# Kernel optimization log

Measured on AMD Instinct MI355X. Metric: run time of the kernel, lower is better.

## Reference

```python
import jax, jax.numpy as jnp
import numpy as np

BN_EPS = 1e-5
INTERP_EPS = 1e-8


def _bn_relu(x, g, b, m, v):
    # eval-mode BatchNorm1d over channel dim (last axis here) + ReLU
    return jax.nn.relu((x - m) * (g / jnp.sqrt(v + BN_EPS)) + b)


def setup_inputs() -> dict:
    key = jax.random.key(0)
    ks = jax.random.split(key, 12)
    B, N, S, C1, C2 = 4, 16384, 1024, 128, 256
    Cin = C1 + C2  # 384
    H1, H2 = 256, 128
    inp = {
        "xyz1": jax.random.normal(ks[0], (B, N, 3), jnp.float32),
        "xyz2": jax.random.normal(ks[1], (B, S, 3), jnp.float32),
        "points1": jax.random.normal(ks[2], (B, N, C1), jnp.float32),
        "points2": jax.random.normal(ks[3], (B, S, C2), jnp.float32),
        # Conv1d(k=1, bias=False) weights: (out_ch, in_ch)
        "w1": jax.random.normal(ks[4], (H1, Cin), jnp.float32) * (1.0 / np.sqrt(Cin)),
        "g1": jax.random.uniform(ks[5], (H1,), jnp.float32, 0.5, 1.5),
        "b1": jax.random.normal(ks[6], (H1,), jnp.float32) * 0.1,
        "m1": jax.random.normal(ks[7], (H1,), jnp.float32) * 0.1,
        "v1": jax.random.uniform(ks[8], (H1,), jnp.float32, 0.5, 1.5),
        "w2": jax.random.normal(ks[9], (H2, H1), jnp.float32) * (1.0 / np.sqrt(H1)),
        "g2": jax.random.uniform(ks[10], (H2,), jnp.float32, 0.5, 1.5),
        "b2": jax.random.normal(ks[11], (H2,), jnp.float32) * 0.1,
        "m2": jnp.zeros((H2,), jnp.float32),
        "v2": jnp.ones((H2,), jnp.float32),
    }
    return inp


def reference(xyz1, xyz2, points1, points2, w1, g1, b1, m1, v1, w2, g2, b2, m2, v2):
    B, N, _ = xyz1.shape
    S = xyz2.shape[1]
    # squared pairwise distances (B, N, S) via ||a||^2 + ||b||^2 - 2 a.b
    sq = (
        jnp.sum(xyz1 * xyz1, -1)[:, :, None]
        + jnp.sum(xyz2 * xyz2, -1)[:, None, :]
        - 2.0 * jnp.einsum("bnd,bsd->bns", xyz1, xyz2)
    )
    neg_d, idx = jax.lax.top_k(-sq, 3)  # 3 nearest neighbors
    dists = -neg_d  # (B, N, 3) squared distances, ascending
    recip = 1.0 / (dists + INTERP_EPS)
    weight = recip / jnp.sum(recip, -1, keepdims=True)  # (B, N, 3)
    # gather neighbor features: (B, N, 3, C2)
    gathered = points2[jnp.arange(B)[:, None, None], idx]
    interpolated = jnp.einsum("bnk,bnkc->bnc", weight, gathered)
    new_points = jnp.concatenate([points1, interpolated], axis=-1)  # (B, N, Cin)
    h = _bn_relu(jnp.einsum("bnc,dc->bnd", new_points, w1), g1, b1, m1, v1)
    out = _bn_relu(jnp.einsum("bnc,dc->bnd", h, w2), g2, b2, m2, v2)
    return out
```

## Files before the change

kernel.cpp:

```cpp
#include <hip/hip_runtime.h>
#include <math.h>

#define B_    4
#define N_    16384
#define S_    1024
#define C1_   128
#define C2_   256
#define CIN_  384
#define H1_   256
#define H2_   128
#define BN_EPS_     1e-5f
#define INTERP_EPS_ 1e-8f

typedef _Float16 f16;
typedef _Float16 f16x4 __attribute__((ext_vector_type(4)));
typedef _Float16 f16x8 __attribute__((ext_vector_type(8)));
typedef float    f32x4 __attribute__((ext_vector_type(4)));
typedef unsigned int u32;

#define GLD16(g, l) \
  __builtin_amdgcn_global_load_lds((const __attribute__((address_space(1))) void*)(g), \
                                   (__attribute__((address_space(3))) void*)(l), 16, 0, 0)

#define WS_XI   1048576
#define WS_W1F  68157440
#define WS_W2F  68354048
#define WS_SC1  68419584
#define WS_SH1  68420608
#define WS_SC2  68421632
#define WS_SH2  68422144

__device__ __forceinline__ u32 umin_(u32 a, u32 b) { return a < b ? a : b; }
__device__ __forceinline__ u32 umax_(u32 a, u32 b) { return a > b ? a : b; }

#define KINS(k) do { \
    u32 c1 = umax_(s0, (k)); s0 = umin_(s0, (k)); \
    u32 c2 = umax_(s1, c1);  s1 = umin_(s1, c1);  \
    u32 c3 = umax_(s2, c2);  s2 = umin_(s2, c2);  \
    u32 c4 = umax_(s3, c3);  s3 = umin_(s3, c3);  \
    s4 = umin_(s4, c4); } while (0)

#define CSWAP(a_, b_) do { \
    if (rd[b_] < rd[a_] || (rd[b_] == rd[a_] && ri[b_] < ri[a_])) { \
      double td = rd[a_]; rd[a_] = rd[b_]; rd[b_] = td; \
      int ti = ri[a_]; ri[a_] = ri[b_]; ri[b_] = ti; } } while (0)

__global__ __launch_bounds__(256) void front_kernel(
    const float* __restrict__ xyz1, const float* __restrict__ xyz2,
    const float* __restrict__ points2,
    const float* __restrict__ w1, const float* __restrict__ w2,
    const float* __restrict__ g1, const float* __restrict__ b1,
    const float* __restrict__ m1, const float* __restrict__ v1,
    const float* __restrict__ g2, const float* __restrict__ b2,
    const float* __restrict__ m2, const float* __restrict__ v2,
    f16* __restrict__ xi, f16* __restrict__ w1f, f16* __restrict__ w2f,
    float* __restrict__ sc1, float* __restrict__ sh1,
    float* __restrict__ sc2, float* __restrict__ sh2)
{
    const int bid = blockIdx.x;
    const int t   = threadIdx.x;

    if (bid >= 2048) {
        const int tg = (bid - 2048) * 256 + t;
        if (tg < 98304) {
            w1f[tg] = (f16)w1[tg];
        } else if (tg < 131072) {
            w2f[tg - 98304] = (f16)w2[tg - 98304];
        } else if (tg < 131328) {
            const int c = tg - 131072;
            const float s = g1[c] / sqrtf(v1[c] + BN_EPS_);
            sc1[c] = s; sh1[c] = b1[c] - m1[c] * s;
        } else if (tg < 131456) {
            const int c = tg - 131328;
            const float s = g2[c] / sqrtf(v2[c] + BN_EPS_);
            sc2[c] = s; sh2[c] = b2[c] - m2[c] * s;
        }
        return;
    }

    __shared__ float4 q[S_ + 8];
    __shared__ int   idr[32][3];
    __shared__ float wtr[32][3];

    const int b     = bid >> 9;
    const int pbase = (bid & 511) << 5;

    for (int i = t; i < S_; i += 256) {
        const float* s = &xyz2[((size_t)b * S_ + i) * 3];
        float4 v; v.x = s[0]; v.y = s[1]; v.z = s[2]; v.w = 0.0f;
        q[i + (i >> 7)] = v;
    }
    __syncthreads();

    {
        const int p     = pbase + (t >> 3);
        const int chunk = t & 7;
        const int qb    = chunk * 129;
        const int ebase = chunk << 7;
        const float* pp = &xyz1[((size_t)b * N_ + p) * 3];
        const float px = pp[0], py = pp[1], pz = pp[2];

        u32 s0 = 0xFFFFFFFFu, s1 = 0xFFFFFFFFu, s2 = 0xFFFFFFFFu,
            s3 = 0xFFFFFFFFu, s4 = 0xFFFFFFFFu;

        for (int i = 0; i < 128; i += 4) {
            #pragma unroll
            for (int u = 0; u < 4; ++u) {
                const float4 c = q[qb + i + u];
                const float dx = px - c.x, dy = py - c.y, dz = pz - c.z;
                const float dd = fmaf(dx, dx, fmaf(dy, dy, dz * dz));
                const u32 k = (__float_as_uint(dd) & 0xFFFFFC00u) | (u32)(ebase + i + u);
                KINS(k);
            }
        }
        #pragma unroll
        for (int msk = 1; msk <= 4; msk <<= 1) {
            u32 e0 = __shfl_xor(s0, msk), e1 = __shfl_xor(s1, msk);
            u32 e2 = __shfl_xor(s2, msk), e3 = __shfl_xor(s3, msk);
            u32 e4 = __shfl_xor(s4, msk);
            KINS(e0); KINS(e1); KINS(e2); KINS(e3); KINS(e4);
        }
        if (chunk == 0) {
            const double px6 = px, py6 = py, pz6 = pz;
            double rd[5]; int ri[5];
            const u32 ks[5] = {s0, s1, s2, s3, s4};
            #pragma unroll
            for (int j = 0; j < 5; ++j) {
                const int si = (int)(ks[j] & 1023u); ri[j] = si;
                const float4 c = q[si + (si >> 7)];
                const double dx = px6 - (double)c.x, dy = py6 - (double)c.y, dz = pz6 - (double)c.z;
                rd[j] = dx * dx + dy * dy + dz * dz;
            }
            CSWAP(0,1); CSWAP(1,2); CSWAP(0,1); CSWAP(2,3); CSWAP(1,2);
            CSWAP(0,1); CSWAP(3,4); CSWAP(2,3); CSWAP(1,2); CSWAP(0,1);
            const float r0 = 1.0f / ((float)rd[0] + INTERP_EPS_);
            const float r1 = 1.0f / ((float)rd[1] + INTERP_EPS_);
            const float r2 = 1.0f / ((float)rd[2] + INTERP_EPS_);
            const float rs = r0 + r1 + r2;
            const int r = t >> 3;
            idr[r][0] = ri[0]; idr[r][1] = ri[1]; idr[r][2] = ri[2];
            wtr[r][0] = r0 / rs; wtr[r][1] = r1 / rs; wtr[r][2] = r2 / rs;
        }
    }
    __syncthreads();

    {
        const int r = t >> 3, j = t & 7;
        const int i0 = idr[r][0], i1 = idr[r][1], i2 = idr[r][2];
        const float w0 = wtr[r][0], w1w = wtr[r][1], w2w = wtr[r][2];
        const float* p2b = points2 + (size_t)b * S_ * C2_;
        const int c0 = j * 32;
        float a[32];
        #pragma unroll
        for (int g = 0; g < 8; ++g) {
            const float4 f = *(const float4*)&p2b[i0 * C2_ + c0 + g * 4];
            a[g*4+0] = w0 * f.x; a[g*4+1] = w0 * f.y; a[g*4+2] = w0 * f.z; a[g*4+3] = w0 * f.w;
        }
        #pragma unroll
        for (int g = 0; g < 8; ++g) {
            const float4 f = *(const float4*)&p2b[i1 * C2_ + c0 + g * 4];
            a[g*4+0] = fmaf(w1w, f.x, a[g*4+0]); a[g*4+1] = fmaf(w1w, f.y, a[g*4+1]);
            a[g*4+2] = fmaf(w1w, f.z, a[g*4+2]); a[g*4+3] = fmaf(w1w, f.w, a[g*4+3]);
        }
        #pragma unroll
        for (int g = 0; g < 8; ++g) {
            const float4 f = *(const float4*)&p2b[i2 * C2_ + c0 + g * 4];
            a[g*4+0] = fmaf(w2w, f.x, a[g*4+0]); a[g*4+1] = fmaf(w2w, f.y, a[g*4+1]);
            a[g*4+2] = fmaf(w2w, f.z, a[g*4+2]); a[g*4+3] = fmaf(w2w, f.w, a[g*4+3]);
        }
        const size_t grow = (size_t)(b * N_ + pbase + r);
        #pragma unroll
        for (int g8 = 0; g8 < 4; ++g8) {
            f16x8 o;
            #pragma unroll
            for (int e = 0; e < 8; ++e) o[e] = (f16)a[g8 * 8 + e];
            *(f16x8*)&xi[grow * C2_ + c0 + g8 * 8] = o;
        }
    }
}

__device__ __forceinline__ void mfma_step1(const f16* As, const f16* Bs,
                                           f32x4 (&acc)[4][8],
                                           int wr, int wc, int lrow, int lhi)
{
    f16x8 af[4], bf[8];
    #pragma unroll
    for (int m = 0; m < 4; ++m)
        af[m] = *(const f16x8*)&As[(wr * 64 + m * 16 + lrow) * 32 + lhi * 8];
    #pragma unroll
    for (int n = 0; n < 8; ++n)
        bf[n] = *(const f16x8*)&Bs[(wc * 128 + n * 16 + lrow) * 32 + lhi * 8];
    #pragma unroll
    for (int m = 0; m < 4; ++m)
        #pragma unroll
        for (int n = 0; n < 8; ++n)
            acc[m][n] = __builtin_amdgcn_mfma_f32_16x16x32_f16(af[m], bf[n], acc[m][n], 0, 0, 0);
}

__global__ __launch_bounds__(256, 2) void mlp_kernel(
    const float* __restrict__ points1, const f16* __restrict__ xi,
    const f16* __restrict__ w1f, const f16* __restrict__ w2f,
    const float* __restrict__ sc1v, const float* __restrict__ sh1v,
    const float* __restrict__ sc2v, const float* __restrict__ sh2v,
    float* __restrict__ out)
{
    extern __shared__ __align__(16) char smem[];
    f16* As = (f16*)smem;
    f16* Bs = (f16*)(smem + 16384);
    char* Ht = smem + 16384;

    const int t = threadIdx.x;
    const int w = t >> 6;
    const int lane = t & 63;
    const int wr = w >> 1, wc = w & 1;
    const int lrow = lane & 15, lhi = lane >> 4;
    const int rowbase = blockIdx.x * 128;

    const int srow = t >> 1, khalf = t & 1;
    const float* p1r = points1 + (size_t)(rowbase + srow) * C1_;

    f32x4 acc[4][8] = {};
    float4 pre0, pre1, pre2, pre3;

    {
        const float* src = p1r + khalf * 16;
        pre0 = *(const float4*)(src + 0);
        pre1 = *(const float4*)(src + 4);
        pre2 = *(const float4*)(src + 8);
        pre3 = *(const float4*)(src + 12);
        f16* asrow = As + srow * 32 + khalf * 16;
        f16x4 o0 = {(f16)pre0.x, (f16)pre0.y, (f16)pre0.z, (f16)pre0.w};
        f16x4 o1 = {(f16)pre1.x, (f16)pre1.y, (f16)pre1.z, (f16)pre1.w};
        f16x4 o2 = {(f16)pre2.x, (f16)pre2.y, (f16)pre2.z, (f16)pre2.w};
        f16x4 o3 = {(f16)pre3.x, (f16)pre3.y, (f16)pre3.z, (f16)pre3.w};
        *(f16x4*)(asrow + 0) = o0; *(f16x4*)(asrow + 4) = o1;
        *(f16x4*)(asrow + 8) = o2; *(f16x4*)(asrow + 12) = o3;
        #pragma unroll
        for (int j = 0; j < 4; ++j) {
            const int c = j * 256 + t;
            GLD16(w1f + (size_t)(c >> 2) * CIN_ + (c & 3) * 8,
                  (char*)Bs + (j * 4096 + w * 1024));
        }
    }
    __syncthreads();

    for (int step = 0; step < 12; ++step) {
        const int pb = step & 1, nb = pb ^ 1;
        const int nkb = (step + 1) * 32;
        const bool has_next = (step < 11);
        const bool nextA = (nkb < C1_);

        if (has_next) {
            if (nextA) {
                const float* src = p1r + nkb + khalf * 16;
                pre0 = *(const float4*)(src + 0);
                pre1 = *(const float4*)(src + 4);
                pre2 = *(const float4*)(src + 8);
                pre3 = *(const float4*)(src + 12);
            } else {
                const int kk = nkb - C1_;
                #pragma unroll
                for (int j = 0; j < 2; ++j) {
                    const int c = j * 256 + t;
                    GLD16(xi + (size_t)(rowbase + (c >> 2)) * C2_ + kk + (c & 3) * 8,
                          (char*)As + (nb * 8192 + j * 4096 + w * 1024));
                }
            }
            #pragma unroll
            for (int j = 0; j < 4; ++j) {
                const int c = j * 256 + t;
                GLD16(w1f + (size_t)(c >> 2) * CIN_ + nkb + (c & 3) * 8,
                      (char*)Bs + (nb * 16384 + j * 4096 + w * 1024));
            }
        }

        mfma_step1(As + pb * 4096, Bs + pb * 8192, acc, wr, wc, lrow, lhi);

        if (has_next && nextA) {
            f16* asrow = As + nb * 4096 + srow * 32 + khalf * 16;
            f16x4 o0 = {(f16)pre0.x, (f16)pre0.y, (f16)pre0.z, (f16)pre0.w};
            f16x4 o1 = {(f16)pre1.x, (f16)pre1.y, (f16)pre1.z, (f16)pre1.w};
            f16x4 o2 = {(f16)pre2.x, (f16)pre2.y, (f16)pre2.z, (f16)pre2.w};
            f16x4 o3 = {(f16)pre3.x, (f16)pre3.y, (f16)pre3.z, (f16)pre3.w};
            *(f16x4*)(asrow + 0) = o0; *(f16x4*)(asrow + 4) = o1;
            *(f16x4*)(asrow + 8) = o2; *(f16x4*)(asrow + 12) = o3;
        }
        __syncthreads();
    }

    #pragma unroll
    for (int j = 0; j < 2; ++j) {
        const int c = j * 256 + t;
        GLD16(w2f + (size_t)(c >> 2) * H1_ + (c & 3) * 8,
              smem + (j * 4096 + w * 1024));
    }
    #pragma unroll
    for (int n = 0; n < 8; ++n) {
        const int col = wc * 128 + n * 16 + lrow;
        const float sc = sc1v[col], sh = sh1v[col];
        #pragma unroll
        for (int m = 0; m < 4; ++m) {
            #pragma unroll
            for (int i = 0; i < 4; ++i) {
                const int row = wr * 64 + m * 16 + lhi * 4 + i;
                const float v = fmaxf(fmaf(acc[m][n][i], sc, sh), 0.0f);
                const u32 byteoff = (u32)(row * 512 + col * 2) ^ ((u32)(row & 7) << 4);
                *(f16*)(Ht + byteoff) = (f16)v;
            }
        }
    }
    __syncthreads();

    f32x4 acc2[4][4] = {};
    for (int step = 0; step < 8; ++step) {
        const int pb = step & 1, nb = pb ^ 1;
        const int nkb = (step + 1) * 32;
        if (step < 7) {
            #pragma unroll
            for (int j = 0; j < 2; ++j) {
                const int c = j * 256 + t;
                GLD16(w2f + (size_t)(c >> 2) * H1_ + nkb + (c & 3) * 8,
                      smem + (nb * 8192 + j * 4096 + w * 1024));
            }
        }
        f16x8 af[4], bf[4];
        #pragma unroll
        for (int m = 0; m < 4; ++m) {
            const int row = wr * 64 + m * 16 + lrow;
            const u32 byteoff = (u32)(row * 512 + (step * 32 + lhi * 8) * 2) ^ ((u32)(row & 7) << 4);
            af[m] = *(const f16x8*)(Ht + byteoff);
        }
        const f16* Bc = (const f16*)(smem + pb * 8192);
        #pragma unroll
        for (int n = 0; n < 4; ++n)
            bf[n] = *(const f16x8*)&Bc[(wc * 64 + n * 16 + lrow) * 32 + lhi * 8];
        #pragma unroll
        for (int m = 0; m < 4; ++m)
            #pragma unroll
            for (int n = 0; n < 4; ++n)
                acc2[m][n] = __builtin_amdgcn_mfma_f32_16x16x32_f16(af[m], bf[n], acc2[m][n], 0, 0, 0);
        __syncthreads();
    }

    #pragma unroll
    for (int n = 0; n < 4; ++n) {
        const int col = wc * 64 + n * 16 + lrow;
        const float sc = sc2v[col], sh = sh2v[col];
        #pragma unroll
        for (int m = 0; m < 4; ++m) {
            const int row0 = rowbase + wr * 64 + m * 16 + lhi * 4;
            #pragma unroll
            for (int i = 0; i < 4; ++i) {
                out[(size_t)(row0 + i) * H2_ + col] = fmaxf(fmaf(acc2[m][n][i], sc, sh), 0.0f);
            }
        }
    }
}

extern "C" void kernel_launch(void* const* d_in, const int* in_sizes, int n_in,
                              void* d_out, int out_size, void* d_ws, size_t ws_size,
                              hipStream_t stream) {
    const float* xyz1    = (const float*)d_in[0];
    const float* xyz2    = (const float*)d_in[1];
    const float* points1 = (const float*)d_in[2];
    const float* points2 = (const float*)d_in[3];
    const float* w1      = (const float*)d_in[4];
    const float* g1      = (const float*)d_in[5];
    const float* b1      = (const float*)d_in[6];
    const float* m1      = (const float*)d_in[7];
    const float* v1      = (const float*)d_in[8];
    const float* w2      = (const float*)d_in[9];
    const float* g2      = (const float*)d_in[10];
    const float* b2      = (const float*)d_in[11];
    const float* m2      = (const float*)d_in[12];
    const float* v2      = (const float*)d_in[13];
    float* out = (float*)d_out;

    char* ws = (char*)d_ws;
    f16*   xi_ws = (f16*)(ws + WS_XI);
    f16*   w1f   = (f16*)(ws + WS_W1F);
    f16*   w2f   = (f16*)(ws + WS_W2F);
    float* sc1   = (float*)(ws + WS_SC1);
    float* sh1   = (float*)(ws + WS_SH1);
    float* sc2   = (float*)(ws + WS_SC2);
    float* sh2   = (float*)(ws + WS_SH2);

    front_kernel<<<dim3(2562), dim3(256), 0, stream>>>(
        xyz1, xyz2, points2, w1, w2, g1, b1, m1, v1, g2, b2, m2, v2,
        xi_ws, w1f, w2f, sc1, sh1, sc2, sh2);
    mlp_kernel<<<dim3(512), dim3(256), 81920, stream>>>(
        points1, xi_ws, w1f, w2f, sc1, sh1, sc2, sh2, out);
}
```

Baseline: 183.9 us.

## Halve MLP row tile and widen KNN per-thread scan range

The front kernel now handles 64 query points per block, with 4 threads per point each scanning 256 candidates instead of 8 threads scanning 128, so fewer blocks reload xyz2 into shared memory and the top-k merge needs fewer shuffle rounds. The MLP kernel drops from 128 to 64 rows per block, cutting shared memory from 80KB to 48KB and accumulators in half so three blocks can fit per CU, and the grid doubles to 1024 blocks. The trade-off is that each W1/W2 tile loaded from global memory is reused across fewer rows, and the longer serial scan per thread in the KNN phase gives less parallelism per point.

```diff
diff --git a/kernel.cpp b/kernel.cpp
--- a/kernel.cpp
+++ b/kernel.cpp
@@ -60,8 +60,8 @@
     const int bid = blockIdx.x;
     const int t   = threadIdx.x;
 
-    if (bid >= 2048) {
-        const int tg = (bid - 2048) * 256 + t;
+    if (bid >= 1024) {
+        const int tg = (bid - 1024) * 256 + t;
         if (tg < 98304) {
             w1f[tg] = (f16)w1[tg];
         } else if (tg < 131072) {
@@ -78,32 +78,32 @@
         return;
     }
 
-    __shared__ float4 q[S_ + 8];
-    __shared__ int   idr[32][3];
-    __shared__ float wtr[32][3];
-
-    const int b     = bid >> 9;
-    const int pbase = (bid & 511) << 5;
+    __shared__ float4 q[S_ + 4];
+    __shared__ int   idr[64][3];
+    __shared__ float wtr[64][3];
+
+    const int b     = bid >> 8;
+    const int pbase = (bid & 255) << 6;
 
     for (int i = t; i < S_; i += 256) {
         const float* s = &xyz2[((size_t)b * S_ + i) * 3];
         float4 v; v.x = s[0]; v.y = s[1]; v.z = s[2]; v.w = 0.0f;
-        q[i + (i >> 7)] = v;
+        q[i + (i >> 8)] = v;
     }
     __syncthreads();
 
     {
-        const int p     = pbase + (t >> 3);
-        const int chunk = t & 7;
-        const int qb    = chunk * 129;
-        const int ebase = chunk << 7;
+        const int p     = pbase + (t >> 2);
+        const int chunk = t & 3;
+        const int qb    = chunk * 257;
+        const int ebase = chunk << 8;
         const float* pp = &xyz1[((size_t)b * N_ + p) * 3];
         const float px = pp[0], py = pp[1], pz = pp[2];
 
         u32 s0 = 0xFFFFFFFFu, s1 = 0xFFFFFFFFu, s2 = 0xFFFFFFFFu,
             s3 = 0xFFFFFFFFu, s4 = 0xFFFFFFFFu;
 
-        for (int i = 0; i < 128; i += 4) {
+        for (int i = 0; i < 256; i += 4) {
             #pragma unroll
             for (int u = 0; u < 4; ++u) {
                 const float4 c = q[qb + i + u];
@@ -114,7 +114,7 @@
             }
         }
         #pragma unroll
-        for (int msk = 1; msk <= 4; msk <<= 1) {
+        for (int msk = 1; msk <= 2; msk <<= 1) {
             u32 e0 = __shfl_xor(s0, msk), e1 = __shfl_xor(s1, msk);
             u32 e2 = __shfl_xor(s2, msk), e3 = __shfl_xor(s3, msk);
             u32 e4 = __shfl_xor(s4, msk);
@@ -127,7 +127,7 @@
             #pragma unroll
             for (int j = 0; j < 5; ++j) {
                 const int si = (int)(ks[j] & 1023u); ri[j] = si;
-                const float4 c = q[si + (si >> 7)];
+                const float4 c = q[si + (si >> 8)];
                 const double dx = px6 - (double)c.x, dy = py6 - (double)c.y, dz = pz6 - (double)c.z;
                 rd[j] = dx * dx + dy * dy + dz * dz;
             }
@@ -137,15 +137,16 @@
             const float r1 = 1.0f / ((float)rd[1] + INTERP_EPS_);
             const float r2 = 1.0f / ((float)rd[2] + INTERP_EPS_);
             const float rs = r0 + r1 + r2;
-            const int r = t >> 3;
+            const int r = t >> 2;
             idr[r][0] = ri[0]; idr[r][1] = ri[1]; idr[r][2] = ri[2];
             wtr[r][0] = r0 / rs; wtr[r][1] = r1 / rs; wtr[r][2] = r2 / rs;
         }
     }
     __syncthreads();
 
-    {
-        const int r = t >> 3, j = t & 7;
+    #pragma unroll
+    for (int rr = 0; rr < 64; rr += 32) {
+        const int r = (t >> 3) + rr, j = t & 7;
         const int i0 = idr[r][0], i1 = idr[r][1], i2 = idr[r][2];
         const float w0 = wtr[r][0], w1w = wtr[r][1], w2w = wtr[r][2];
         const float* p2b = points2 + (size_t)b * S_ * C2_;
@@ -179,25 +180,7 @@
     }
 }
 
-__device__ __forceinline__ void mfma_step1(const f16* As, const f16* Bs,
-                                           f32x4 (&acc)[4][8],
-                                           int wr, int wc, int lrow, int lhi)
-{
-    f16x8 af[4], bf[8];
-    #pragma unroll
-    for (int m = 0; m < 4; ++m)
-        af[m] = *(const f16x8*)&As[(wr * 64 + m * 16 + lrow) * 32 + lhi * 8];
-    #pragma unroll
-    for (int n = 0; n < 8; ++n)
-        bf[n] = *(const f16x8*)&Bs[(wc * 128 + n * 16 + lrow) * 32 + lhi * 8];
-    #pragma unroll
-    for (int m = 0; m < 4; ++m)
-        #pragma unroll
-        for (int n = 0; n < 8; ++n)
-            acc[m][n] = __builtin_amdgcn_mfma_f32_16x16x32_f16(af[m], bf[n], acc[m][n], 0, 0, 0);
-}
-
-__global__ __launch_bounds__(256, 2) void mlp_kernel(
+__global__ __launch_bounds__(256, 3) void mlp_kernel(
     const float* __restrict__ points1, const f16* __restrict__ xi,
     const f16* __restrict__ w1f, const f16* __restrict__ w2f,
     const float* __restrict__ sc1v, const float* __restrict__ sh1v,
@@ -206,7 +189,7 @@
 {
     extern __shared__ __align__(16) char smem[];
     f16* As = (f16*)smem;
-    f16* Bs = (f16*)(smem + 16384);
+    f16* Bs = (f16*)(smem + 8192);
     char* Ht = smem + 16384;
 
     const int t = threadIdx.x;
@@ -214,27 +197,22 @@
     const int lane = t & 63;
     const int wr = w >> 1, wc = w & 1;
     const int lrow = lane & 15, lhi = lane >> 4;
-    const int rowbase = blockIdx.x * 128;
-
-    const int srow = t >> 1, khalf = t & 1;
+    const int rowbase = blockIdx.x * 64;
+
+    const int srow = t >> 2, kq = t & 3;
     const float* p1r = points1 + (size_t)(rowbase + srow) * C1_;
 
-    f32x4 acc[4][8] = {};
-    float4 pre0, pre1, pre2, pre3;
+    f32x4 acc[2][8] = {};
+    float4 pre0, pre1;
 
     {
-        const float* src = p1r + khalf * 16;
+        const float* src = p1r + kq * 8;
         pre0 = *(const float4*)(src + 0);
         pre1 = *(const float4*)(src + 4);
-        pre2 = *(const float4*)(src + 8);
-        pre3 = *(const float4*)(src + 12);
-        f16* asrow = As + srow * 32 + khalf * 16;
+        f16* asrow = As + srow * 32 + kq * 8;
         f16x4 o0 = {(f16)pre0.x, (f16)pre0.y, (f16)pre0.z, (f16)pre0.w};
         f16x4 o1 = {(f16)pre1.x, (f16)pre1.y, (f16)pre1.z, (f16)pre1.w};
-        f16x4 o2 = {(f16)pre2.x, (f16)pre2.y, (f16)pre2.z, (f16)pre2.w};
-        f16x4 o3 = {(f16)pre3.x, (f16)pre3.y, (f16)pre3.z, (f16)pre3.w};
         *(f16x4*)(asrow + 0) = o0; *(f16x4*)(asrow + 4) = o1;
-        *(f16x4*)(asrow + 8) = o2; *(f16x4*)(asrow + 12) = o3;
         #pragma unroll
         for (int j = 0; j < 4; ++j) {
             const int c = j * 256 + t;
@@ -252,19 +230,13 @@
 
         if (has_next) {
             if (nextA) {
-                const float* src = p1r + nkb + khalf * 16;
+                const float* src = p1r + nkb + kq * 8;
                 pre0 = *(const float4*)(src + 0);
                 pre1 = *(const float4*)(src + 4);
-                pre2 = *(const float4*)(src + 8);
-                pre3 = *(const float4*)(src + 12);
             } else {
                 const int kk = nkb - C1_;
-                #pragma unroll
-                for (int j = 0; j < 2; ++j) {
-                    const int c = j * 256 + t;
-                    GLD16(xi + (size_t)(rowbase + (c >> 2)) * C2_ + kk + (c & 3) * 8,
-                          (char*)As + (nb * 8192 + j * 4096 + w * 1024));
-                }
+                GLD16(xi + (size_t)(rowbase + (t >> 2)) * C2_ + kk + (t & 3) * 8,
+                      (char*)As + (nb * 4096 + w * 1024));
             }
             #pragma unroll
             for (int j = 0; j < 4; ++j) {
@@ -274,16 +246,28 @@
             }
         }
 
-        mfma_step1(As + pb * 4096, Bs + pb * 8192, acc, wr, wc, lrow, lhi);
+        {
+            const f16* Ac = As + pb * 2048;
+            const f16* Bc = Bs + pb * 8192;
+            f16x8 af[2], bf[8];
+            #pragma unroll
+            for (int m = 0; m < 2; ++m)
+                af[m] = *(const f16x8*)&Ac[(wr * 32 + m * 16 + lrow) * 32 + lhi * 8];
+            #pragma unroll
+            for (int n = 0; n < 8; ++n)
+                bf[n] = *(const f16x8*)&Bc[(wc * 128 + n * 16 + lrow) * 32 + lhi * 8];
+            #pragma unroll
+            for (int m = 0; m < 2; ++m)
+                #pragma unroll
+                for (int n = 0; n < 8; ++n)
+                    acc[m][n] = __builtin_amdgcn_mfma_f32_16x16x32_f16(af[m], bf[n], acc[m][n], 0, 0, 0);
+        }
 
         if (has_next && nextA) {
-            f16* asrow = As + nb * 4096 + srow * 32 + khalf * 16;
+            f16* asrow = As + nb * 2048 + srow * 32 + kq * 8;
             f16x4 o0 = {(f16)pre0.x, (f16)pre0.y, (f16)pre0.z, (f16)pre0.w};
             f16x4 o1 = {(f16)pre1.x, (f16)pre1.y, (f16)pre1.z, (f16)pre1.w};
-            f16x4 o2 = {(f16)pre2.x, (f16)pre2.y, (f16)pre2.z, (f16)pre2.w};
-            f16x4 o3 = {(f16)pre3.x, (f16)pre3.y, (f16)pre3.z, (f16)pre3.w};
             *(f16x4*)(asrow + 0) = o0; *(f16x4*)(asrow + 4) = o1;
-            *(f16x4*)(asrow + 8) = o2; *(f16x4*)(asrow + 12) = o3;
         }
         __syncthreads();
     }
@@ -299,10 +283,10 @@
         const int col = wc * 128 + n * 16 + lrow;
         const float sc = sc1v[col], sh = sh1v[col];
         #pragma unroll
-        for (int m = 0; m < 4; ++m) {
+        for (int m = 0; m < 2; ++m) {
             #pragma unroll
             for (int i = 0; i < 4; ++i) {
-                const int row = wr * 64 + m * 16 + lhi * 4 + i;
+                const int row = wr * 32 + m * 16 + lhi * 4 + i;
                 const float v = fmaxf(fmaf(acc[m][n][i], sc, sh), 0.0f);
                 const u32 byteoff = (u32)(row * 512 + col * 2) ^ ((u32)(row & 7) << 4);
                 *(f16*)(Ht + byteoff) = (f16)v;
@@ -311,7 +295,7 @@
     }
     __syncthreads();
 
-    f32x4 acc2[4][4] = {};
+    f32x4 acc2[2][4] = {};
     for (int step = 0; step < 8; ++step) {
         const int pb = step & 1, nb = pb ^ 1;
         const int nkb = (step + 1) * 32;
@@ -323,10 +307,10 @@
                       smem + (nb * 8192 + j * 4096 + w * 1024));
             }
         }
-        f16x8 af[4], bf[4];
-        #pragma unroll
-        for (int m = 0; m < 4; ++m) {
-            const int row = wr * 64 + m * 16 + lrow;
+        f16x8 af[2], bf[4];
+        #pragma unroll
+        for (int m = 0; m < 2; ++m) {
+            const int row = wr * 32 + m * 16 + lrow;
             const u32 byteoff = (u32)(row * 512 + (step * 32 + lhi * 8) * 2) ^ ((u32)(row & 7) << 4);
             af[m] = *(const f16x8*)(Ht + byteoff);
         }
@@ -335,7 +319,7 @@
         for (int n = 0; n < 4; ++n)
             bf[n] = *(const f16x8*)&Bc[(wc * 64 + n * 16 + lrow) * 32 + lhi * 8];
         #pragma unroll
-        for (int m = 0; m < 4; ++m)
+        for (int m = 0; m < 2; ++m)
             #pragma unroll
             for (int n = 0; n < 4; ++n)
                 acc2[m][n] = __builtin_amdgcn_mfma_f32_16x16x32_f16(af[m], bf[n], acc2[m][n], 0, 0, 0);
@@ -347,8 +331,8 @@
         const int col = wc * 64 + n * 16 + lrow;
         const float sc = sc2v[col], sh = sh2v[col];
         #pragma unroll
-        for (int m = 0; m < 4; ++m) {
-            const int row0 = rowbase + wr * 64 + m * 16 + lhi * 4;
+        for (int m = 0; m < 2; ++m) {
+            const int row0 = rowbase + wr * 32 + m * 16 + lhi * 4;
             #pragma unroll
             for (int i = 0; i < 4; ++i) {
                 out[(size_t)(row0 + i) * H2_ + col] = fmaxf(fmaf(acc2[m][n][i], sc, sh), 0.0f);
@@ -385,9 +369,9 @@
     float* sc2   = (float*)(ws + WS_SC2);
     float* sh2   = (float*)(ws + WS_SH2);
 
-    front_kernel<<<dim3(2562), dim3(256), 0, stream>>>(
+    front_kernel<<<dim3(1538), dim3(256), 0, stream>>>(
         xyz1, xyz2, points2, w1, w2, g1, b1, m1, v1, g2, b2, m2, v2,
         xi_ws, w1f, w2f, sc1, sh1, sc2, sh2);
-    mlp_kernel<<<dim3(512), dim3(256), 81920, stream>>>(
+    mlp_kernel<<<dim3(1024), dim3(256), 49152, stream>>>(
         points1, xi_ws, w1f, w2f, sc1, sh1, sc2, sh2, out);
 }
```

Result: slower. 193.6 us (+5.2%).
